# Performance work log

Hardware: AMD Instinct MI355X
Metric: run time of the kernel (lower is better)

## Reference

```python
import jax, jax.numpy as jnp
import numpy as np

N = 8192        # nodes
NFEAT = 256     # input feature dim
NHID = 64       # per-head hidden dim
NHEADS = 4
NCLASS = 121    # PPI label count
ALPHA = 0.2     # LeakyReLU negative slope
NEG_INF = jnp.float32(-9e15)  # pyGAT's mask fill value


def setup_inputs() -> dict:
    key = jax.random.key(0)
    k = jax.random.split(key, 6)
    x = jax.random.normal(k[0], (N, NFEAT), dtype=jnp.float32)
    adj = (jax.random.uniform(k[1], (N, N)) < 0.01).astype(jnp.float32)
    idx = jnp.arange(N)
    adj = adj.at[idx, idx].set(1.0)
    # per-head first-layer params: W [H, nfeat, nhid], a [H, 2*nhid]
    Ws = jax.random.normal(k[2], (NHEADS, NFEAT, NHID), dtype=jnp.float32) * 0.1
    a_heads = jax.random.normal(k[3], (NHEADS, 2 * NHID), dtype=jnp.float32) * 0.1
    # output attention layer params
    W_out = jax.random.normal(k[4], (NHEADS * NHID, NCLASS), dtype=jnp.float32) * 0.1
    a_out = jax.random.normal(k[5], (2 * NCLASS,), dtype=jnp.float32) * 0.1
    return {"x": x, "adj": adj, "Ws": Ws, "a_heads": a_heads,
            "W_out": W_out, "a_out": a_out}


def _gat_head(x, adj, W, a, concat):
    # Dense GraphAttentionLayer (pyGAT), eval mode (dropout off).
    Wh = x @ W                                   # [N, d]
    d = W.shape[1]
    f_src = Wh @ a[:d]                           # [N]  score contribution of node i
    f_dst = Wh @ a[d:]                           # [N]  score contribution of node j
    e = jax.nn.leaky_relu(f_src[:, None] + f_dst[None, :], ALPHA)  # [N, N]
    e = jnp.where(adj > 0, e, NEG_INF)
    att = jax.nn.softmax(e, axis=-1)             # [N, N]
    h = att @ Wh                                 # [N, d]
    return jax.nn.elu(h) if concat else h


def reference(x, adj, Ws, a_heads, W_out, a_out):
    # first multi-head layer (concat=True, elu), vmapped over heads
    heads = jax.vmap(lambda W, a: _gat_head(x, adj, W, a, True))(Ws, a_heads)  # [H, N, nhid]
    h_cat = jnp.transpose(heads, (1, 0, 2)).reshape(x.shape[0], NHEADS * NHID)  # torch.cat(dim=1)
    # output attention layer (concat=False -> raw aggregation)
    return _gat_head(h_cat, adj, W_out, a_out, False)  # [N, nclass]
```

## Files before the change

### kernel.cpp

```cpp
#include <hip/hip_runtime.h>
#include <math.h>

#define N_NODES 8192
#define NFEAT 256
#define NHID 64
#define NHEADS 4
#define NCLASS 121
#define NCPAD 128
#define CAP 256
#define LRALPHA 0.2f

__global__ __launch_bounds__(256) void build_csr(const float* __restrict__ adj,
                                                 int* __restrict__ nbr,
                                                 int* __restrict__ deg) {
    int row = blockIdx.x;
    __shared__ int cnt;
    if (threadIdx.x == 0) cnt = 0;
    __syncthreads();
    const float4* arow = (const float4*)(adj + (size_t)row * N_NODES);
    for (int j4 = threadIdx.x; j4 < N_NODES / 4; j4 += 256) {
        float4 v = arow[j4];
        if (v.x > 0.f) { int s = atomicAdd(&cnt, 1); if (s < CAP) nbr[row * CAP + s] = j4 * 4 + 0; }
        if (v.y > 0.f) { int s = atomicAdd(&cnt, 1); if (s < CAP) nbr[row * CAP + s] = j4 * 4 + 1; }
        if (v.z > 0.f) { int s = atomicAdd(&cnt, 1); if (s < CAP) nbr[row * CAP + s] = j4 * 4 + 2; }
        if (v.w > 0.f) { int s = atomicAdd(&cnt, 1); if (s < CAP) nbr[row * CAP + s] = j4 * 4 + 3; }
    }
    __syncthreads();
    if (threadIdx.x == 0) deg[row] = cnt < CAP ? cnt : CAP;
}

__global__ __launch_bounds__(256) void pad_params(const float* __restrict__ Wout,
                                                  const float* __restrict__ aout,
                                                  float* __restrict__ Wpad,
                                                  float* __restrict__ apad) {
    int idx = blockIdx.x * 256 + threadIdx.x;
    if (idx < 256 * NCPAD) {
        int k = idx >> 7, c = idx & 127;
        Wpad[idx] = (c < NCLASS) ? Wout[k * NCLASS + c] : 0.f;
    }
    if (idx < 256) {
        int c = idx & 127;
        float v = 0.f;
        if (c < NCLASS) v = (idx < 128) ? aout[c] : aout[NCLASS + c];
        apad[idx] = v;
    }
}

__global__ __launch_bounds__(256) void gemm1(const float* __restrict__ x,
                                             const float* __restrict__ Ws,
                                             float* __restrict__ Wh1) {
    int h = blockIdx.y;
    int r0 = blockIdx.x * 64;
    __shared__ float xs[64][260];
    for (int t = threadIdx.x; t < 64 * 64; t += 256) {
        int r = t >> 6, c4 = t & 63;
        *(float4*)&xs[r][c4 * 4] = *(const float4*)(x + (size_t)(r0 + r) * NFEAT + c4 * 4);
    }
    __syncthreads();
    int d = threadIdx.x & 63;
    int rb = (threadIdx.x >> 6) * 16;
    const float* W = Ws + (size_t)h * NFEAT * NHID + d;
    float acc[16] = {};
    for (int k4 = 0; k4 < NFEAT; k4 += 4) {
        float b0 = W[(k4 + 0) * NHID];
        float b1 = W[(k4 + 1) * NHID];
        float b2 = W[(k4 + 2) * NHID];
        float b3 = W[(k4 + 3) * NHID];
#pragma unroll
        for (int r = 0; r < 16; r++) {
            float4 a = *(const float4*)&xs[rb + r][k4];
            acc[r] += a.x * b0 + a.y * b1 + a.z * b2 + a.w * b3;
        }
    }
#pragma unroll
    for (int r = 0; r < 16; r++)
        Wh1[((size_t)(r0 + rb + r) * NHEADS + h) * NHID + d] = acc[r];
}

__global__ __launch_bounds__(256) void attn_coef1(const float* __restrict__ Wh1,
                                                  const float* __restrict__ a_heads,
                                                  float* __restrict__ fs1,
                                                  float* __restrict__ fd1) {
    int i = blockIdx.x;
    int h = threadIdx.x >> 6, lane = threadIdx.x & 63;
    float wh = Wh1[((size_t)i * NHEADS + h) * NHID + lane];
    float s = wh * a_heads[h * 2 * NHID + lane];
    float dd = wh * a_heads[h * 2 * NHID + NHID + lane];
#pragma unroll
    for (int o = 32; o > 0; o >>= 1) { s += __shfl_down(s, o); dd += __shfl_down(dd, o); }
    if (lane == 0) { fs1[h * N_NODES + i] = s; fd1[h * N_NODES + i] = dd; }
}

__global__ __launch_bounds__(256) void attn_agg1(const int* __restrict__ nbr,
                                                 const int* __restrict__ deg,
                                                 const float* __restrict__ Wh1,
                                                 const float* __restrict__ fs1,
                                                 const float* __restrict__ fd1,
                                                 float* __restrict__ hcat) {
    int i = blockIdx.x;
    int h = threadIdx.x >> 6, lane = threadIdx.x & 63;
    __shared__ float ebuf[NHEADS][CAP];
    __shared__ int nbrs[CAP];
    int dg = deg[i];
    for (int t = threadIdx.x; t < dg; t += 256) nbrs[t] = nbr[i * CAP + t];
    __syncthreads();
    float fsi = fs1[h * N_NODES + i];
    const float* fdh = fd1 + h * N_NODES;
    float m = -3.4e38f;
    for (int t = lane; t < dg; t += 64) {
        float e = fsi + fdh[nbrs[t]];
        e = e > 0.f ? e : LRALPHA * e;
        ebuf[h][t] = e;
        m = fmaxf(m, e);
    }
#pragma unroll
    for (int o = 32; o > 0; o >>= 1) m = fmaxf(m, __shfl_xor(m, o));
    float s = 0.f;
    for (int t = lane; t < dg; t += 64) {
        float p = __expf(ebuf[h][t] - m);
        ebuf[h][t] = p;
        s += p;
    }
#pragma unroll
    for (int o = 32; o > 0; o >>= 1) s += __shfl_xor(s, o);
    __syncthreads();
    float acc = 0.f;
    const float* whh = Wh1 + h * NHID + lane;
    for (int t = 0; t < dg; t++) {
        int j = nbrs[t];
        acc += ebuf[h][t] * whh[(size_t)j * (NHEADS * NHID)];
    }
    acc /= s;
    float r = acc > 0.f ? acc : expm1f(acc);
    hcat[(size_t)i * (NHEADS * NHID) + h * NHID + lane] = r;
}

__global__ __launch_bounds__(256) void gemm2(const float* __restrict__ hcat,
                                             const float* __restrict__ Wpad,
                                             float* __restrict__ Wh2) {
    int r0 = blockIdx.x * 64;
    __shared__ float xs[64][260];
    for (int t = threadIdx.x; t < 64 * 64; t += 256) {
        int r = t >> 6, c4 = t & 63;
        *(float4*)&xs[r][c4 * 4] = *(const float4*)(hcat + (size_t)(r0 + r) * 256 + c4 * 4);
    }
    __syncthreads();
    int c0 = (threadIdx.x & 63) * 2;
    int rb = (threadIdx.x >> 6) * 16;
    float acc0[16] = {}, acc1[16] = {};
    for (int k4 = 0; k4 < 256; k4 += 4) {
        float2 b0 = *(const float2*)&Wpad[(k4 + 0) * NCPAD + c0];
        float2 b1 = *(const float2*)&Wpad[(k4 + 1) * NCPAD + c0];
        float2 b2 = *(const float2*)&Wpad[(k4 + 2) * NCPAD + c0];
        float2 b3 = *(const float2*)&Wpad[(k4 + 3) * NCPAD + c0];
#pragma unroll
        for (int r = 0; r < 16; r++) {
            float4 a = *(const float4*)&xs[rb + r][k4];
            acc0[r] += a.x * b0.x + a.y * b1.x + a.z * b2.x + a.w * b3.x;
            acc1[r] += a.x * b0.y + a.y * b1.y + a.z * b2.y + a.w * b3.y;
        }
    }
#pragma unroll
    for (int r = 0; r < 16; r++) {
        float2 v = make_float2(acc0[r], acc1[r]);
        *(float2*)&Wh2[(size_t)(r0 + rb + r) * NCPAD + c0] = v;
    }
}

__global__ __launch_bounds__(256) void attn_coef2(const float* __restrict__ Wh2,
                                                  const float* __restrict__ apad,
                                                  float* __restrict__ fs2,
                                                  float* __restrict__ fd2) {
    int i = blockIdx.x * 4 + (threadIdx.x >> 6);
    int lane = threadIdx.x & 63;
    float w0 = Wh2[(size_t)i * NCPAD + lane];
    float w1 = Wh2[(size_t)i * NCPAD + 64 + lane];
    float s = w0 * apad[lane] + w1 * apad[64 + lane];
    float dd = w0 * apad[128 + lane] + w1 * apad[192 + lane];
#pragma unroll
    for (int o = 32; o > 0; o >>= 1) { s += __shfl_down(s, o); dd += __shfl_down(dd, o); }
    if (lane == 0) { fs2[i] = s; fd2[i] = dd; }
}

__global__ __launch_bounds__(128) void attn_agg2(const int* __restrict__ nbr,
                                                 const int* __restrict__ deg,
                                                 const float* __restrict__ Wh2,
                                                 const float* __restrict__ fs2,
                                                 const float* __restrict__ fd2,
                                                 float* __restrict__ out) {
    int i = blockIdx.x;
    int t = threadIdx.x;
    __shared__ float ebuf[CAP];
    __shared__ int nbrs[CAP];
    __shared__ float red[2];
    int dg = deg[i];
    for (int u = t; u < dg; u += 128) nbrs[u] = nbr[i * CAP + u];
    __syncthreads();
    float fsi = fs2[i];
    float m = -3.4e38f;
    for (int u = t; u < dg; u += 128) {
        float e = fsi + fd2[nbrs[u]];
        e = e > 0.f ? e : LRALPHA * e;
        ebuf[u] = e;
        m = fmaxf(m, e);
    }
#pragma unroll
    for (int o = 32; o > 0; o >>= 1) m = fmaxf(m, __shfl_xor(m, o));
    if ((t & 63) == 0) red[t >> 6] = m;
    __syncthreads();
    m = fmaxf(red[0], red[1]);
    float s = 0.f;
    for (int u = t; u < dg; u += 128) {
        float p = __expf(ebuf[u] - m);
        ebuf[u] = p;
        s += p;
    }
#pragma unroll
    for (int o = 32; o > 0; o >>= 1) s += __shfl_xor(s, o);
    __syncthreads();
    if ((t & 63) == 0) red[t >> 6] = s;
    __syncthreads();
    s = red[0] + red[1];
    float acc = 0.f;
    const float* wcol = Wh2 + t;
    for (int u = 0; u < dg; u++) {
        acc += ebuf[u] * wcol[(size_t)nbrs[u] * NCPAD];
    }
    if (t < NCLASS) out[(size_t)i * NCLASS + t] = acc / s;
}


extern "C" void kernel_launch(void* const* d_in, const int* in_sizes, int n_in,
                              void* d_out, int out_size, void* d_ws, size_t ws_size,
                              hipStream_t stream) {
    const float* x       = (const float*)d_in[0];
    const float* adj     = (const float*)d_in[1];
    const float* Ws      = (const float*)d_in[2];
    const float* a_heads = (const float*)d_in[3];
    const float* Wout    = (const float*)d_in[4];
    const float* aout    = (const float*)d_in[5];
    float* out = (float*)d_out;

    char* ws = (char*)d_ws;
    size_t off = 0;
    auto alloc = [&](size_t bytes) { void* p = ws + off; off = (off + bytes + 255) & ~(size_t)255; return p; };
    int*   nbr  = (int*)  alloc((size_t)N_NODES * CAP * 4);
    int*   deg  = (int*)  alloc((size_t)N_NODES * 4);
    float* Wh1  = (float*)alloc((size_t)N_NODES * NHEADS * NHID * 4);
    float* fs1  = (float*)alloc((size_t)NHEADS * N_NODES * 4);
    float* fd1  = (float*)alloc((size_t)NHEADS * N_NODES * 4);
    float* hcat = (float*)alloc((size_t)N_NODES * NHEADS * NHID * 4);
    float* Wh2  = (float*)alloc((size_t)N_NODES * NCPAD * 4);
    float* fs2  = (float*)alloc((size_t)N_NODES * 4);
    float* fd2  = (float*)alloc((size_t)N_NODES * 4);
    float* Wpad = (float*)alloc((size_t)256 * NCPAD * 4);
    float* apad = (float*)alloc((size_t)256 * 4);

    build_csr<<<N_NODES, 256, 0, stream>>>(adj, nbr, deg);
    pad_params<<<128, 256, 0, stream>>>(Wout, aout, Wpad, apad);
    gemm1<<<dim3(N_NODES / 64, NHEADS), 256, 0, stream>>>(x, Ws, Wh1);
    attn_coef1<<<N_NODES, 256, 0, stream>>>(Wh1, a_heads, fs1, fd1);
    attn_agg1<<<N_NODES, 256, 0, stream>>>(nbr, deg, Wh1, fs1, fd1, hcat);
    gemm2<<<N_NODES / 64, 256, 0, stream>>>(hcat, Wpad, Wh2);
    attn_coef2<<<N_NODES / 4, 256, 0, stream>>>(Wh2, apad, fs2, fd2);
    attn_agg2<<<N_NODES, 128, 0, stream>>>(nbr, deg, Wh2, fs2, fd2, out);
}
```

Before: 529.1 us.

## Split neighbor aggregation across waves with vectorized row gathers and smem reduction

Both attention aggregation kernels now split the neighbor list across the block's four waves instead of having one thread loop over all neighbors per output dimension. Each wave gathers full feature rows with float4/float2 loads, two neighbors per iteration, and partial sums are then combined through shared memory. The goal is to shorten the serial dependent-load chain and increase memory-level parallelism in the gathers. The cost is extra shared memory and one more block barrier. attn_agg2 also moves to 256 threads.

```diff
diff --git a/kernel.cpp b/kernel.cpp
--- a/kernel.cpp
+++ b/kernel.cpp
@@ -99,8 +99,10 @@
                                                  float* __restrict__ hcat) {
     int i = blockIdx.x;
     int h = threadIdx.x >> 6, lane = threadIdx.x & 63;
-    __shared__ float ebuf[NHEADS][CAP];
+    __shared__ float ebuf[NHEADS][CAP + 1];
     __shared__ int nbrs[CAP];
+    __shared__ float inv_s[NHEADS];
+    __shared__ float part[NHEADS][256];
     int dg = deg[i];
     for (int t = threadIdx.x; t < dg; t += 256) nbrs[t] = nbr[i * CAP + t];
     __syncthreads();
@@ -123,16 +125,33 @@
     }
 #pragma unroll
     for (int o = 32; o > 0; o >>= 1) s += __shfl_xor(s, o);
-    __syncthreads();
-    float acc = 0.f;
-    const float* whh = Wh1 + h * NHID + lane;
-    for (int t = 0; t < dg; t++) {
+    if (lane == 0) inv_s[h] = 1.f / s;
+    __syncthreads();
+    int w = h;
+    int hh = lane >> 4;
+    float4 acc = make_float4(0.f, 0.f, 0.f, 0.f);
+    int t = w;
+    for (; t + 8 <= dg; t += 8) {
+        int j0 = nbrs[t], j1 = nbrs[t + 4];
+        float4 v0 = ((const float4*)(Wh1 + (size_t)j0 * 256))[lane];
+        float4 v1 = ((const float4*)(Wh1 + (size_t)j1 * 256))[lane];
+        float p0 = ebuf[hh][t], p1 = ebuf[hh][t + 4];
+        acc.x += p0 * v0.x; acc.y += p0 * v0.y; acc.z += p0 * v0.z; acc.w += p0 * v0.w;
+        acc.x += p1 * v1.x; acc.y += p1 * v1.y; acc.z += p1 * v1.z; acc.w += p1 * v1.w;
+    }
+    for (; t < dg; t += 4) {
         int j = nbrs[t];
-        acc += ebuf[h][t] * whh[(size_t)j * (NHEADS * NHID)];
-    }
-    acc /= s;
-    float r = acc > 0.f ? acc : expm1f(acc);
-    hcat[(size_t)i * (NHEADS * NHID) + h * NHID + lane] = r;
+        float4 v = ((const float4*)(Wh1 + (size_t)j * 256))[lane];
+        float p = ebuf[hh][t];
+        acc.x += p * v.x; acc.y += p * v.y; acc.z += p * v.z; acc.w += p * v.w;
+    }
+    ((float4*)part[w])[lane] = acc;
+    __syncthreads();
+    int dim = threadIdx.x;
+    float r = part[0][dim] + part[1][dim] + part[2][dim] + part[3][dim];
+    r *= inv_s[dim >> 6];
+    r = r > 0.f ? r : expm1f(r);
+    hcat[(size_t)i * 256 + dim] = r;
 }
 
 __global__ __launch_bounds__(256) void gemm2(const float* __restrict__ hcat,
@@ -182,51 +201,71 @@
     if (lane == 0) { fs2[i] = s; fd2[i] = dd; }
 }
 
-__global__ __launch_bounds__(128) void attn_agg2(const int* __restrict__ nbr,
+__global__ __launch_bounds__(256) void attn_agg2(const int* __restrict__ nbr,
                                                  const int* __restrict__ deg,
                                                  const float* __restrict__ Wh2,
                                                  const float* __restrict__ fs2,
                                                  const float* __restrict__ fd2,
                                                  float* __restrict__ out) {
     int i = blockIdx.x;
-    int t = threadIdx.x;
+    int w = threadIdx.x >> 6, lane = threadIdx.x & 63;
     __shared__ float ebuf[CAP];
     __shared__ int nbrs[CAP];
-    __shared__ float red[2];
+    __shared__ float red[4];
+    __shared__ float part[4][128];
+    __shared__ float inv_s;
     int dg = deg[i];
-    for (int u = t; u < dg; u += 128) nbrs[u] = nbr[i * CAP + u];
+    for (int t = threadIdx.x; t < dg; t += 256) nbrs[t] = nbr[i * CAP + t];
     __syncthreads();
     float fsi = fs2[i];
     float m = -3.4e38f;
-    for (int u = t; u < dg; u += 128) {
-        float e = fsi + fd2[nbrs[u]];
+    for (int t = threadIdx.x; t < dg; t += 256) {
+        float e = fsi + fd2[nbrs[t]];
         e = e > 0.f ? e : LRALPHA * e;
-        ebuf[u] = e;
+        ebuf[t] = e;
         m = fmaxf(m, e);
     }
 #pragma unroll
     for (int o = 32; o > 0; o >>= 1) m = fmaxf(m, __shfl_xor(m, o));
-    if ((t & 63) == 0) red[t >> 6] = m;
-    __syncthreads();
-    m = fmaxf(red[0], red[1]);
+    if (lane == 0) red[w] = m;
+    __syncthreads();
+    m = fmaxf(fmaxf(red[0], red[1]), fmaxf(red[2], red[3]));
     float s = 0.f;
-    for (int u = t; u < dg; u += 128) {
-        float p = __expf(ebuf[u] - m);
-        ebuf[u] = p;
+    for (int t = threadIdx.x; t < dg; t += 256) {
+        float p = __expf(ebuf[t] - m);
+        ebuf[t] = p;
         s += p;
     }
 #pragma unroll
     for (int o = 32; o > 0; o >>= 1) s += __shfl_xor(s, o);
     __syncthreads();
-    if ((t & 63) == 0) red[t >> 6] = s;
-    __syncthreads();
-    s = red[0] + red[1];
-    float acc = 0.f;
-    const float* wcol = Wh2 + t;
-    for (int u = 0; u < dg; u++) {
-        acc += ebuf[u] * wcol[(size_t)nbrs[u] * NCPAD];
-    }
-    if (t < NCLASS) out[(size_t)i * NCLASS + t] = acc / s;
+    if (lane == 0) red[w] = s;
+    __syncthreads();
+    if (threadIdx.x == 0) inv_s = 1.f / (red[0] + red[1] + red[2] + red[3]);
+    __syncthreads();
+    float2 acc = make_float2(0.f, 0.f);
+    int t = w;
+    for (; t + 8 <= dg; t += 8) {
+        int j0 = nbrs[t], j1 = nbrs[t + 4];
+        float2 v0 = ((const float2*)(Wh2 + (size_t)j0 * NCPAD))[lane];
+        float2 v1 = ((const float2*)(Wh2 + (size_t)j1 * NCPAD))[lane];
+        float p0 = ebuf[t], p1 = ebuf[t + 4];
+        acc.x += p0 * v0.x; acc.y += p0 * v0.y;
+        acc.x += p1 * v1.x; acc.y += p1 * v1.y;
+    }
+    for (; t < dg; t += 4) {
+        int j = nbrs[t];
+        float2 v = ((const float2*)(Wh2 + (size_t)j * NCPAD))[lane];
+        float p = ebuf[t];
+        acc.x += p * v.x; acc.y += p * v.y;
+    }
+    ((float2*)part[w])[lane] = acc;
+    __syncthreads();
+    if (threadIdx.x < NCPAD) {
+        int dim = threadIdx.x;
+        float r = (part[0][dim] + part[1][dim] + part[2][dim] + part[3][dim]) * inv_s;
+        if (dim < NCLASS) out[(size_t)i * NCLASS + dim] = r;
+    }
 }
 
 
@@ -263,5 +302,5 @@
     attn_agg1<<<N_NODES, 256, 0, stream>>>(nbr, deg, Wh1, fs1, fd1, hcat);
     gemm2<<<N_NODES / 64, 256, 0, stream>>>(hcat, Wpad, Wh2);
     attn_coef2<<<N_NODES / 4, 256, 0, stream>>>(Wh2, apad, fs2, fd2);
-    attn_agg2<<<N_NODES, 128, 0, stream>>>(nbr, deg, Wh2, fs2, fd2, out);
-}
+    attn_agg2<<<N_NODES, 256, 0, stream>>>(nbr, deg, Wh2, fs2, fd2, out);
+}
```

Result: no change. 532.8 us (+0.7%).
